# Kernel optimization log

Measured on AMD Instinct MI355X. Metric: run time of the kernel, lower is better.

## Reference

```python
import jax, jax.numpy as jnp
import numpy as np

C, FF, NH = 128, 2048, 8
B, D, H, W = 1, 16, 16, 16
EPS = 1e-5

def setup_inputs() -> dict:
    key = jax.random.key(0)
    ks = jax.random.split(key, 20)
    s = 0.02
    inp = {
        'x': jax.random.normal(ks[0], (B, C, D, H, W), jnp.float32),
        'Wq': jax.random.normal(ks[1], (C, C), jnp.float32) * s,
        'bq': jnp.zeros((C,), jnp.float32),
        'Wk': jax.random.normal(ks[2], (C, C), jnp.float32) * s,
        'bk': jnp.zeros((C,), jnp.float32),
        'Wv': jax.random.normal(ks[3], (C, C), jnp.float32) * s,
        'bv': jnp.zeros((C,), jnp.float32),
        'Wo': jax.random.normal(ks[4], (C, C), jnp.float32) * s,
        'bo': jnp.zeros((C,), jnp.float32),
        'W1': jax.random.normal(ks[5], (FF, C), jnp.float32) * s,
        'b1': jnp.zeros((FF,), jnp.float32),
        'W2': jax.random.normal(ks[6], (C, FF), jnp.float32) * s,
        'b2': jnp.zeros((C,), jnp.float32),
        'g1': jnp.ones((C,), jnp.float32),
        'be1': jnp.zeros((C,), jnp.float32),
        'g2': jnp.ones((C,), jnp.float32),
        'be2': jnp.zeros((C,), jnp.float32),
    }
    return inp

def _layernorm(t, g, b):
    # normalize over last (channel) dim, biased variance like torch LayerNorm
    m = jnp.mean(t, axis=-1, keepdims=True)
    v = jnp.mean(jnp.square(t - m), axis=-1, keepdims=True)
    return (t - m) * jax.lax.rsqrt(v + EPS) * g + b

def reference(x, Wq, bq, Wk, bk, Wv, bv, Wo, bo, W1, b1, W2, b2, g1, be1, g2, be2):
    b_, c, d, h, w = x.shape
    n = d * h * w
    hd = c // NH
    xf = x.reshape(b_, c, n)  # [B,C,N]
    # 1x1 conv3d == per-voxel linear over channels
    q = jnp.einsum('oc,bcn->bon', Wq, xf) + bq[:, None]
    k = jnp.einsum('oc,bcn->bon', Wk, xf) + bk[:, None]
    v = jnp.einsum('oc,bcn->bon', Wv, xf) + bv[:, None]
    q = q.reshape(b_, NH, hd, n)
    k = k.reshape(b_, NH, hd, n)
    v = v.reshape(b_, NH, hd, n)
    scores = jnp.einsum('bhcd,bhce->bhde', q, k) / (hd ** 0.5)  # [B,NH,N,N]
    probs = jax.nn.softmax(scores, axis=-1)
    attn = jnp.einsum('bhde,bhce->bhcd', probs, v).reshape(b_, c, n)
    attn = jnp.einsum('oc,bcn->bon', Wo, attn) + bo[:, None]
    x1 = xf + attn  # residual (dropout = identity at eval)
    x1 = _layernorm(x1.transpose(0, 2, 1), g1, be1)  # [B,N,C]
    hmid = jax.nn.relu(jnp.einsum('fc,bnc->bnf', W1, x1) + b1)
    ffn = jnp.einsum('cf,bnf->bnc', W2, hmid) + b2
    x2 = _layernorm(x1 + ffn, g2, be2)
    return x2.transpose(0, 2, 1).reshape(b_, c, d, h, w)
```

## Files before the change

kernel.cpp:

```cpp
#include <hip/hip_runtime.h>
#include <hip/hip_bf16.h>

typedef __hip_bfloat16 bf16;
typedef short short8 __attribute__((ext_vector_type(8)));
typedef float f32x4 __attribute__((ext_vector_type(4)));
typedef unsigned int u32x4 __attribute__((ext_vector_type(4)));

#define C_   128
#define N_   4096
#define NH_  8
#define HD_  16
#define FF_  2048
#define SCALE_Q 0.360673760222241f

__device__ __forceinline__ unsigned short f2bf_bits(float f) {
    bf16 h = __float2bfloat16(f);
    return *reinterpret_cast<unsigned short*>(&h);
}
__device__ __forceinline__ unsigned int pack_trunc(float lo, float hi) {
    return __builtin_amdgcn_perm(__float_as_uint(hi), __float_as_uint(lo), 0x07060302u);
}
__device__ __forceinline__ short f2bf_trunc(float f) {
    return (short)(__float_as_uint(f) >> 16);
}
__device__ __forceinline__ float bfs2f(short s) {
    return __uint_as_float(((unsigned int)(unsigned short)s) << 16);
}
__device__ __forceinline__ float fast_exp2(float x) {
    return __builtin_amdgcn_exp2f(x);
}
__device__ __forceinline__ f32x4 mfma16(short8 a, short8 b, f32x4 c) {
    return __builtin_amdgcn_mfma_f32_16x16x32_bf16(a, b, c, 0, 0, 0);
}

__global__ void __launch_bounds__(256) k_prep(
    const float* __restrict__ Wq, const float* __restrict__ Wk,
    const float* __restrict__ Wv, const float* __restrict__ Wo,
    const float* __restrict__ W1, const float* __restrict__ W2,
    const float* __restrict__ x,
    bf16* __restrict__ Wqkvf, bf16* __restrict__ Wof,
    bf16* __restrict__ W1f, bf16* __restrict__ W2f,
    bf16* __restrict__ xTf)
{
    const int i = blockIdx.x * 256 + threadIdx.x;
    if (i < 73728) {
        const float* row;
        bf16* dst;
        int kblk, g;
        if (i < 8192) {
            const int o = i >> 4;
            kblk = (i >> 2) & 3; g = i & 3;
            const int odx = (o < 384) ? o : o - 384;
            row = (o < 128) ? (Wq + o * 128)
                : (o < 256) ? (Wk + (o - 128) * 128)
                : (o < 384) ? (Wv + (o - 256) * 128)
                            : (Wo + (o - 384) * 128);
            bf16* buf = (o < 384) ? Wqkvf : Wof;
            dst = buf + ((((odx >> 4) << 2) + kblk) * 512 + ((g << 4) + (odx & 15)) * 8);
        } else if (i < 40960) {
            const int t = i - 8192, o = t >> 4;
            kblk = (t >> 2) & 3; g = t & 3;
            row = W1 + o * 128;
            dst = W1f + ((((o >> 4) << 2) + kblk) * 512 + ((g << 4) + (o & 15)) * 8);
        } else {
            const int t = i - 40960, o = t >> 8;
            kblk = (t >> 2) & 63; g = t & 3;
            row = W2 + o * 2048;
            dst = W2f + ((((o >> 4) << 6) + kblk) * 512 + ((g << 4) + (o & 15)) * 8);
        }
        const int k0 = kblk * 32 + g * 4;
        const f32x4 lo = *(const f32x4*)(row + k0);
        const f32x4 hi = *(const f32x4*)(row + k0 + 16);
        u32x4 w;
        #pragma unroll
        for (int j = 0; j < 4; ++j)
            w[j] = ((unsigned int)f2bf_bits(hi[j]) << 16) | f2bf_bits(lo[j]);
        *(u32x4*)dst = w;
    } else {
        const int t = i - 73728;
        const int n = t & 4095, g = (t >> 12) & 3, cblk = t >> 14;
        const int c0 = cblk * 32 + g * 4;
        const float* xs = x + (size_t)c0 * 4096 + n;
        u32x4 w;
        #pragma unroll
        for (int j = 0; j < 4; ++j)
            w[j] = ((unsigned int)f2bf_bits(xs[(size_t)(16 + j) * 4096]) << 16)
                 | f2bf_bits(xs[(size_t)j * 4096]);
        bf16* dst = xTf + ((((n >> 4) << 2) + cblk) * 512 + ((g << 4) + (n & 15)) * 8);
        *(u32x4*)dst = w;
    }
}

__global__ void __launch_bounds__(256) k_qkv(
    const bf16* __restrict__ xTf, const bf16* __restrict__ Wqkvf,
    const float* __restrict__ bq, const float* __restrict__ bk, const float* __restrict__ bv,
    bf16* __restrict__ qf, bf16* __restrict__ kf, bf16* __restrict__ vf)
{
    const int tid = threadIdx.x, wave = tid >> 6, lane = tid & 63;
    const int col = lane & 15, quad = lane >> 4;
    const int gw = blockIdx.x * 4 + wave;
    const int rt = gw / 24, ct = gw % 24;
    f32x4 acc = {};
    #pragma unroll
    for (int c = 0; c < 4; ++c) {
        short8 a = *(const short8*)(xTf + ((size_t)(rt * 4 + c) << 9) + lane * 8);
        short8 b = *(const short8*)(Wqkvf + ((size_t)(ct * 4 + c) << 9) + lane * 8);
        acc = mfma16(a, b, acc);
    }
    #pragma unroll
    for (int r = 0; r < 4; ++r) {
        const int m = rt * 16 + quad * 4 + r;
        const int n = ct * 16 + col;
        const float v = acc[r];
        if (n < 128) {
            const int h = n >> 4, ch = n & 15;
            qf[((h << 8) + (m >> 4)) * 256 + (((ch >> 3) << 4) + (m & 15)) * 8 + (ch & 7)] =
                __float2bfloat16((v + bq[n]) * SCALE_Q);
        } else if (n < 256) {
            const int c2 = n - 128, h = c2 >> 4, ch = c2 & 15;
            kf[((h << 8) + (m >> 4)) * 256 + (((ch >> 3) << 4) + (m & 15)) * 8 + (ch & 7)] =
                __float2bfloat16(v + bk[c2]);
        } else {
            const int c2 = n - 256, h = c2 >> 4, ch = c2 & 15;
            const int ko = m & 31;
            const int pos = ((ko & 15) << 1) + (ko >> 4);
            vf[((h << 7) + (m >> 5)) * 512 + (((pos >> 3) << 4) + ch) * 8 + (pos & 7)] =
                __float2bfloat16(v + bv[c2]);
        }
    }
}

__global__ void __launch_bounds__(256)
attn_kernel(const bf16* __restrict__ qf, const bf16* __restrict__ kf,
            const bf16* __restrict__ vf, bf16* __restrict__ af)
{
    __shared__ __align__(16) union {
        unsigned int P[4][4][2][320];
        float comb[4][4][64][8];
    } sh;
    const int tid = threadIdx.x, wave = tid >> 6, lane = tid & 63;
    const int col = lane & 15, quad = lane >> 4;
    const int gw = blockIdx.x;
    const int h  = gw >> 6;
    const int tile0 = (gw & 63) << 2;
    const f32x4 zero = {};

    short8 aq[4] = {{}, {}, {}, {}};
    if (quad < 2) {
        #pragma unroll
        for (int qt = 0; qt < 4; ++qt)
            aq[qt] = *(const short8*)(qf + ((size_t)((h << 8) + tile0 + qt) << 8) + lane * 8);
    }

    const short8 onesb = { (short)0x3F80, (short)0x3F80, (short)0x3F80, (short)0x3F80,
                           (short)0x3F80, (short)0x3F80, (short)0x3F80, (short)0x3F80 };

    f32x4 accO[4] = {{}, {}, {}, {}};
    f32x4 accL[4] = {{}, {}, {}, {}};

    const int kbeg = wave << 10;

    for (int i = 0; i < 32; i += 2) {
        const int mA = kbeg + (i << 5);
        const int mB = mA + 32;

        short8 bkA0 = {}, bkA1 = {}, bkB0 = {}, bkB1 = {};
        if (quad < 2) {
            const bf16* ka = kf + ((size_t)((h << 8) + (mA >> 4)) << 8) + lane * 8;
            bkA0 = *(const short8*)(ka);
            bkA1 = *(const short8*)(ka + 256);
            bkB0 = *(const short8*)(ka + 512);
            bkB1 = *(const short8*)(ka + 768);
        }
        const short8 vA = *(const short8*)(vf + ((size_t)((h << 7) + (mA >> 5)) << 9) + lane * 8);
        const short8 vB = *(const short8*)(vf + ((size_t)((h << 7) + (mB >> 5)) << 9) + lane * 8);

        #pragma unroll
        for (int qt = 0; qt < 4; ++qt) {
            f32x4 s0 = mfma16(aq[qt], bkA0, zero);
            f32x4 s1 = mfma16(aq[qt], bkA1, zero);
            f32x4 s2 = mfma16(aq[qt], bkB0, zero);
            f32x4 s3 = mfma16(aq[qt], bkB1, zero);
            unsigned int* P0 = &sh.P[wave][qt][0][0];
            unsigned int* P1 = &sh.P[wave][qt][1][0];
            #pragma unroll
            for (int r = 0; r < 4; ++r) {
                P0[(quad * 4 + r) * 20 + col] = pack_trunc(fast_exp2(s0[r]), fast_exp2(s1[r]));
                P1[(quad * 4 + r) * 20 + col] = pack_trunc(fast_exp2(s2[r]), fast_exp2(s3[r]));
            }
        }
        #pragma unroll
        for (int qt = 0; qt < 4; ++qt) {
            const short* Ps0 = (const short*)&sh.P[wave][qt][0][0];
            const short* Ps1 = (const short*)&sh.P[wave][qt][1][0];
            short8 ap0 = *(const short8*)(Ps0 + col * 40 + quad * 8);
            accO[qt] = mfma16(ap0, vA, accO[qt]);
            accL[qt] = mfma16(ap0, onesb, accL[qt]);
            short8 ap1 = *(const short8*)(Ps1 + col * 40 + quad * 8);
            accO[qt] = mfma16(ap1, vB, accO[qt]);
            accL[qt] = mfma16(ap1, onesb, accL[qt]);
        }
    }

    __syncthreads();
    #pragma unroll
    for (int qt = 0; qt < 4; ++qt)
        #pragma unroll
        for (int r = 0; r < 4; ++r) {
            sh.comb[qt][wave][lane][r]     = accO[qt][r];
            sh.comb[qt][wave][lane][4 + r] = accL[qt][r];
        }
    __syncthreads();

    {
        const int qt = wave, tile = tile0 + qt;
        #pragma unroll
        for (int r = 0; r < 4; ++r) {
            float O = sh.comb[qt][0][lane][r] + sh.comb[qt][1][lane][r]
                    + sh.comb[qt][2][lane][r] + sh.comb[qt][3][lane][r];
            float l = sh.comb[qt][0][lane][4+r] + sh.comb[qt][1][lane][4+r]
                    + sh.comb[qt][2][lane][4+r] + sh.comb[qt][3][lane][4+r];
            const int row16 = quad * 4 + r;
            const int pk = (col << 1) + (h & 1);
            af[((tile << 2) + (h >> 1)) * 512 + (((pk >> 3) << 4) + row16) * 8 + (pk & 7)] =
                __float2bfloat16(O / l);
        }
    }
}

__global__ void __launch_bounds__(512, 2)
k_mega(const bf16* __restrict__ af, const bf16* __restrict__ xTf,
       const bf16* __restrict__ Wof, const bf16* __restrict__ W1f, const bf16* __restrict__ W2f,
       const float* __restrict__ bo, const float* __restrict__ b1, const float* __restrict__ b2,
       const float* __restrict__ g1, const float* __restrict__ be1,
       const float* __restrict__ g2, const float* __restrict__ be2,
       float* __restrict__ out)
{
    __shared__ __align__(16) unsigned int Pb[8][2][320];
    __shared__ float comb[224][64];
    const int tid = threadIdx.x, wave = tid >> 6, lane = tid & 63;
    const int col = lane & 15, quad = lane >> 4;
    const int rt = blockIdx.x, n0 = rt << 4;
    const f32x4 zero = {};

    short8 ao[4], xt[4];
    #pragma unroll
    for (int c = 0; c < 4; ++c) {
        ao[c] = *(const short8*)(af  + ((size_t)(rt * 4 + c) << 9) + lane * 8);
        xt[c] = *(const short8*)(xTf + ((size_t)(rt * 4 + c) << 9) + lane * 8);
    }
    f32x4 d[8];
    #pragma unroll
    for (int t = 0; t < 8; ++t) d[t] = zero;
    #pragma unroll
    for (int t = 0; t < 8; ++t)
        #pragma unroll
        for (int c = 0; c < 4; ++c) {
            short8 b = *(const short8*)(Wof + ((size_t)(t * 4 + c) << 9) + lane * 8);
            d[t] = mfma16(ao[c], b, d[t]);
        }
    #pragma unroll
    for (int t = 0; t < 8; ++t) {
        const float bt = bo[t * 16 + col];
        #pragma unroll
        for (int r = 0; r < 4; ++r) d[t][r] += bt;
    }

    float x1f[4][8];
    #pragma unroll
    for (int c = 0; c < 4; ++c) {
        unsigned int* Pw = &Pb[wave][c & 1][0];
        const short* Ps = (const short*)Pw;
        #pragma unroll
        for (int r = 0; r < 4; ++r)
            Pw[(quad * 4 + r) * 20 + col] = pack_trunc(d[2 * c][r], d[2 * c + 1][r]);
        short8 ar = *(const short8*)(Ps + col * 40 + quad * 8);
        #pragma unroll
        for (int j = 0; j < 8; ++j)
            x1f[c][j] = bfs2f(ar[j]) + bfs2f(xt[c][j]);
    }

    float s = 0.f, ss = 0.f;
    #pragma unroll
    for (int c = 0; c < 4; ++c)
        #pragma unroll
        for (int j = 0; j < 8; ++j) { s += x1f[c][j]; ss += x1f[c][j] * x1f[c][j]; }
    s  += __shfl_xor(s, 16);  s  += __shfl_xor(s, 32);
    ss += __shfl_xor(ss, 16); ss += __shfl_xor(ss, 32);
    const float m1 = s * (1.f / 128.f);
    const float rstd1 = rsqrtf(ss * (1.f / 128.f) - m1 * m1 + 1e-5f);
    short8 aq1[4];
    #pragma unroll
    for (int c = 0; c < 4; ++c)
        #pragma unroll
        for (int j = 0; j < 8; ++j) {
            const int pos = quad * 8 + j;
            const int ko = ((pos & 1) << 4) + (pos >> 1);
            const int ch = c * 32 + ko;
            aq1[c][j] = f2bf_trunc((x1f[c][j] - m1) * rstd1 * g1[ch] + be1[ch]);
        }

    f32x4 ACC[8];
    #pragma unroll
    for (int t = 0; t < 8; ++t) ACC[t] = zero;
    for (int i = 0; i < 8; ++i) {
        const int ffc = (wave << 3) + i;
        f32x4 p0 = zero, p1 = zero;
        #pragma unroll
        for (int c = 0; c < 4; ++c) {
            short8 b = *(const short8*)(W1f + ((size_t)(ffc * 8 + c) << 9) + lane * 8);
            p0 = mfma16(aq1[c], b, p0);
        }
        #pragma unroll
        for (int c = 0; c < 4; ++c) {
            short8 b = *(const short8*)(W1f + ((size_t)(ffc * 8 + 4 + c) << 9) + lane * 8);
            p1 = mfma16(aq1[c], b, p1);
        }
        const float bb0 = b1[ffc * 32 + col], bb1 = b1[ffc * 32 + 16 + col];
        unsigned int* Pw = &Pb[wave][i & 1][0];
        #pragma unroll
        for (int r = 0; r < 4; ++r)
            Pw[(quad * 4 + r) * 20 + col] =
                pack_trunc(fmaxf(p0[r] + bb0, 0.f), fmaxf(p1[r] + bb1, 0.f));
        short8 ah = *(const short8*)((const short*)Pw + col * 40 + quad * 8);
        #pragma unroll
        for (int t = 0; t < 8; ++t) {
            short8 bw = *(const short8*)(W2f + ((size_t)(t * 64 + ffc) << 9) + lane * 8);
            ACC[t] = mfma16(ah, bw, ACC[t]);
        }
    }

    if (wave) {
        #pragma unroll
        for (int t = 0; t < 8; ++t)
            #pragma unroll
            for (int r = 0; r < 4; ++r)
                comb[(wave - 1) * 32 + t * 4 + r][lane] = ACC[t][r];
    }
    __syncthreads();
    if (wave == 0) {
        #pragma unroll
        for (int t = 0; t < 8; ++t)
            #pragma unroll
            for (int r = 0; r < 4; ++r) {
                float acc = ACC[t][r];
                #pragma unroll
                for (int w = 0; w < 7; ++w)
                    acc += comb[w * 32 + t * 4 + r][lane];
                ACC[t][r] = acc;
            }
        short* xb = (short*)&Pb[0][0][0];
        #pragma unroll
        for (int c = 0; c < 4; ++c)
            *(short8*)(xb + (col * 4 + c) * 32 + quad * 8) = aq1[c];
        float t2[8][4];
        #pragma unroll
        for (int t = 0; t < 8; ++t) {
            const int ch = t * 16 + col;
            const int pk = (col << 1) + (t & 1);
            const int c = t >> 1;
            const float bb = b2[ch];
            #pragma unroll
            for (int r = 0; r < 4; ++r)
                t2[t][r] = ACC[t][r] + bb + bfs2f(xb[((quad * 4 + r) * 4 + c) * 32 + pk]);
        }
        #pragma unroll
        for (int r = 0; r < 4; ++r) {
            float S = 0.f, SS = 0.f;
            #pragma unroll
            for (int t = 0; t < 8; ++t) { S += t2[t][r]; SS += t2[t][r] * t2[t][r]; }
            S  += __shfl_xor(S, 1);  S  += __shfl_xor(S, 2);
            S  += __shfl_xor(S, 4);  S  += __shfl_xor(S, 8);
            SS += __shfl_xor(SS, 1); SS += __shfl_xor(SS, 2);
            SS += __shfl_xor(SS, 4); SS += __shfl_xor(SS, 8);
            const float m2 = S * (1.f / 128.f);
            const float rstd2 = rsqrtf(SS * (1.f / 128.f) - m2 * m2 + 1e-5f);
            #pragma unroll
            for (int t = 0; t < 8; ++t) {
                const int ch = t * 16 + col;
                out[(size_t)ch * N_ + n0 + quad * 4 + r] =
                    (t2[t][r] - m2) * rstd2 * g2[ch] + be2[ch];
            }
        }
    }
}

extern "C" void kernel_launch(void* const* d_in, const int* in_sizes, int n_in,
                              void* d_out, int out_size, void* d_ws, size_t ws_size,
                              hipStream_t stream) {
    const float* x   = (const float*)d_in[0];
    const float* Wq  = (const float*)d_in[1];
    const float* bq  = (const float*)d_in[2];
    const float* Wk  = (const float*)d_in[3];
    const float* bk  = (const float*)d_in[4];
    const float* Wv  = (const float*)d_in[5];
    const float* bv  = (const float*)d_in[6];
    const float* Wo  = (const float*)d_in[7];
    const float* bo  = (const float*)d_in[8];
    const float* W1  = (const float*)d_in[9];
    const float* b1  = (const float*)d_in[10];
    const float* W2  = (const float*)d_in[11];
    const float* b2  = (const float*)d_in[12];
    const float* g1  = (const float*)d_in[13];
    const float* be1 = (const float*)d_in[14];
    const float* g2  = (const float*)d_in[15];
    const float* be2 = (const float*)d_in[16];
    float* out = (float*)d_out;

    char* ws = (char*)d_ws;
    bf16* xTf   = (bf16*)(ws + 0);
    bf16* qf    = (bf16*)(ws + 1048576);
    bf16* kf    = (bf16*)(ws + 2097152);
    bf16* vf    = (bf16*)(ws + 3145728);
    bf16* af    = (bf16*)(ws + 4194304);
    bf16* Wqkvf = (bf16*)(ws + 5242880);
    bf16* Wof   = (bf16*)(ws + 5341184);
    bf16* W1f   = (bf16*)(ws + 5373952);
    bf16* W2f   = (bf16*)(ws + 5898240);

    k_prep<<<544, 256, 0, stream>>>(Wq, Wk, Wv, Wo, W1, W2, x, Wqkvf, Wof, W1f, W2f, xTf);
    k_qkv<<<1536, 256, 0, stream>>>(xTf, Wqkvf, bq, bk, bv, qf, kf, vf);
    attn_kernel<<<512, 256, 0, stream>>>(qf, kf, vf, af);
    k_mega<<<256, 512, 0, stream>>>(af, xTf, Wof, W1f, W2f, bo, b1, b2,
                                    g1, be1, g2, be2, out);
}
```

Before: 139.2 us.

## Fuse all four kernels into one persistent kernel with grid-wide barriers

Replaces the four separate launches (prep, qkv, attention, mega) with a single persistent kernel of 256 blocks of 512 threads. The stages are separated by atomic-counter grid barriers, and a memset resets the counter before each launch. The W1/W2 weight conversion moves into the QKV stage so it overlaps with that work, and attention now runs two jobs per block. This removes launch gaps and tail effects between kernels, at the cost of barrier spin time, lower occupancy in the attention stage, and reliance on all 256 blocks being co-resident.

```diff
diff --git a/kernel.cpp b/kernel.cpp
--- a/kernel.cpp
+++ b/kernel.cpp
@@ -33,353 +33,379 @@
     return __builtin_amdgcn_mfma_f32_16x16x32_bf16(a, b, c, 0, 0, 0);
 }
 
-__global__ void __launch_bounds__(256) k_prep(
-    const float* __restrict__ Wq, const float* __restrict__ Wk,
-    const float* __restrict__ Wv, const float* __restrict__ Wo,
-    const float* __restrict__ W1, const float* __restrict__ W2,
-    const float* __restrict__ x,
-    bf16* __restrict__ Wqkvf, bf16* __restrict__ Wof,
-    bf16* __restrict__ W1f, bf16* __restrict__ W2f,
-    bf16* __restrict__ xTf)
+__device__ __forceinline__ void grid_sync(unsigned int* bar, unsigned int target) {
+    __syncthreads();
+    if (threadIdx.x == 0) {
+        __hip_atomic_fetch_add(bar, 1u, __ATOMIC_ACQ_REL, __HIP_MEMORY_SCOPE_AGENT);
+        while (__hip_atomic_load(bar, __ATOMIC_ACQUIRE, __HIP_MEMORY_SCOPE_AGENT) < target)
+            __builtin_amdgcn_s_sleep(2);
+    }
+    __syncthreads();
+}
+
+__global__ void __launch_bounds__(512)
+k_fused(const float* __restrict__ x,
+        const float* __restrict__ Wq, const float* __restrict__ Wk,
+        const float* __restrict__ Wv, const float* __restrict__ Wo,
+        const float* __restrict__ W1, const float* __restrict__ W2,
+        const float* __restrict__ bq, const float* __restrict__ bk,
+        const float* __restrict__ bv, const float* __restrict__ bo,
+        const float* __restrict__ b1, const float* __restrict__ b2,
+        const float* __restrict__ g1, const float* __restrict__ be1,
+        const float* __restrict__ g2, const float* __restrict__ be2,
+        bf16* __restrict__ xTf, bf16* __restrict__ Wqkvf, bf16* __restrict__ Wof,
+        bf16* __restrict__ W1f, bf16* __restrict__ W2f,
+        bf16* __restrict__ qf, bf16* __restrict__ kf, bf16* __restrict__ vf,
+        bf16* __restrict__ af,
+        float* __restrict__ out, unsigned int* __restrict__ bar)
 {
-    const int i = blockIdx.x * 256 + threadIdx.x;
-    if (i < 73728) {
-        const float* row;
-        bf16* dst;
-        int kblk, g;
+    __shared__ __align__(16) union {
+        unsigned int P[2][4][4][2][320];
+        float comba[2][4][4][64][8];
+        struct {
+            unsigned int Pb[8][2][320];
+            float comb[224][64];
+        } mg;
+    } sh;
+
+    const int tid  = threadIdx.x, wave = tid >> 6, lane = tid & 63;
+    const int col  = lane & 15,  quad = lane >> 4;
+    const int blk  = blockIdx.x;
+    const f32x4 zero = {};
+
+    {
+        const int i = blk * 512 + tid;
         if (i < 8192) {
             const int o = i >> 4;
-            kblk = (i >> 2) & 3; g = i & 3;
+            const int kblk = (i >> 2) & 3, g = i & 3;
             const int odx = (o < 384) ? o : o - 384;
-            row = (o < 128) ? (Wq + o * 128)
-                : (o < 256) ? (Wk + (o - 128) * 128)
-                : (o < 384) ? (Wv + (o - 256) * 128)
-                            : (Wo + (o - 384) * 128);
+            const float* row = (o < 128) ? (Wq + o * 128)
+                             : (o < 256) ? (Wk + (o - 128) * 128)
+                             : (o < 384) ? (Wv + (o - 256) * 128)
+                                         : (Wo + (o - 384) * 128);
             bf16* buf = (o < 384) ? Wqkvf : Wof;
-            dst = buf + ((((odx >> 4) << 2) + kblk) * 512 + ((g << 4) + (odx & 15)) * 8);
-        } else if (i < 40960) {
-            const int t = i - 8192, o = t >> 4;
-            kblk = (t >> 2) & 3; g = t & 3;
-            row = W1 + o * 128;
-            dst = W1f + ((((o >> 4) << 2) + kblk) * 512 + ((g << 4) + (o & 15)) * 8);
-        } else {
-            const int t = i - 40960, o = t >> 8;
-            kblk = (t >> 2) & 63; g = t & 3;
-            row = W2 + o * 2048;
-            dst = W2f + ((((o >> 4) << 6) + kblk) * 512 + ((g << 4) + (o & 15)) * 8);
-        }
-        const int k0 = kblk * 32 + g * 4;
-        const f32x4 lo = *(const f32x4*)(row + k0);
-        const f32x4 hi = *(const f32x4*)(row + k0 + 16);
-        u32x4 w;
-        #pragma unroll
-        for (int j = 0; j < 4; ++j)
-            w[j] = ((unsigned int)f2bf_bits(hi[j]) << 16) | f2bf_bits(lo[j]);
-        *(u32x4*)dst = w;
-    } else {
-        const int t = i - 73728;
-        const int n = t & 4095, g = (t >> 12) & 3, cblk = t >> 14;
-        const int c0 = cblk * 32 + g * 4;
-        const float* xs = x + (size_t)c0 * 4096 + n;
-        u32x4 w;
-        #pragma unroll
-        for (int j = 0; j < 4; ++j)
-            w[j] = ((unsigned int)f2bf_bits(xs[(size_t)(16 + j) * 4096]) << 16)
-                 | f2bf_bits(xs[(size_t)j * 4096]);
-        bf16* dst = xTf + ((((n >> 4) << 2) + cblk) * 512 + ((g << 4) + (n & 15)) * 8);
-        *(u32x4*)dst = w;
+            bf16* dst = buf + ((((odx >> 4) << 2) + kblk) * 512 + ((g << 4) + (odx & 15)) * 8);
+            const int k0 = kblk * 32 + g * 4;
+            const f32x4 lo = *(const f32x4*)(row + k0);
+            const f32x4 hi = *(const f32x4*)(row + k0 + 16);
+            u32x4 w;
+            #pragma unroll
+            for (int j = 0; j < 4; ++j)
+                w[j] = ((unsigned int)f2bf_bits(hi[j]) << 16) | f2bf_bits(lo[j]);
+            *(u32x4*)dst = w;
+        } else if (i < 73728) {
+            const int t = i - 8192;
+            const int n = t & 4095, g = (t >> 12) & 3, cblk = t >> 14;
+            const int c0 = cblk * 32 + g * 4;
+            const float* xs = x + (size_t)c0 * 4096 + n;
+            u32x4 w;
+            #pragma unroll
+            for (int j = 0; j < 4; ++j)
+                w[j] = ((unsigned int)f2bf_bits(xs[(size_t)(16 + j) * 4096]) << 16)
+                     | f2bf_bits(xs[(size_t)j * 4096]);
+            bf16* dst = xTf + ((((n >> 4) << 2) + cblk) * 512 + ((g << 4) + (n & 15)) * 8);
+            *(u32x4*)dst = w;
+        }
     }
-}
-
-__global__ void __launch_bounds__(256) k_qkv(
-    const bf16* __restrict__ xTf, const bf16* __restrict__ Wqkvf,
-    const float* __restrict__ bq, const float* __restrict__ bk, const float* __restrict__ bv,
-    bf16* __restrict__ qf, bf16* __restrict__ kf, bf16* __restrict__ vf)
-{
-    const int tid = threadIdx.x, wave = tid >> 6, lane = tid & 63;
-    const int col = lane & 15, quad = lane >> 4;
-    const int gw = blockIdx.x * 4 + wave;
-    const int rt = gw / 24, ct = gw % 24;
-    f32x4 acc = {};
-    #pragma unroll
-    for (int c = 0; c < 4; ++c) {
-        short8 a = *(const short8*)(xTf + ((size_t)(rt * 4 + c) << 9) + lane * 8);
-        short8 b = *(const short8*)(Wqkvf + ((size_t)(ct * 4 + c) << 9) + lane * 8);
-        acc = mfma16(a, b, acc);
+
+    grid_sync(bar, 256);
+
+    {
+        const int wv = blk * 8 + wave;
+        #pragma unroll
+        for (int j = 0; j < 3; ++j) {
+            const int gw = j * 2048 + wv;
+            const int rt = gw / 24, ct = gw % 24;
+            f32x4 acc = {};
+            #pragma unroll
+            for (int c = 0; c < 4; ++c) {
+                short8 a = *(const short8*)(xTf + ((size_t)(rt * 4 + c) << 9) + lane * 8);
+                short8 b = *(const short8*)(Wqkvf + ((size_t)(ct * 4 + c) << 9) + lane * 8);
+                acc = mfma16(a, b, acc);
+            }
+            #pragma unroll
+            for (int r = 0; r < 4; ++r) {
+                const int m = rt * 16 + quad * 4 + r;
+                const int n = ct * 16 + col;
+                const float v = acc[r];
+                if (n < 128) {
+                    const int h = n >> 4, ch = n & 15;
+                    qf[((h << 8) + (m >> 4)) * 256 + (((ch >> 3) << 4) + (m & 15)) * 8 + (ch & 7)] =
+                        __float2bfloat16((v + bq[n]) * SCALE_Q);
+                } else if (n < 256) {
+                    const int c2 = n - 128, h = c2 >> 4, ch = c2 & 15;
+                    kf[((h << 8) + (m >> 4)) * 256 + (((ch >> 3) << 4) + (m & 15)) * 8 + (ch & 7)] =
+                        __float2bfloat16(v + bk[c2]);
+                } else {
+                    const int c2 = n - 256, h = c2 >> 4, ch = c2 & 15;
+                    const int ko = m & 31;
+                    const int pos = ((ko & 15) << 1) + (ko >> 4);
+                    vf[((h << 7) + (m >> 5)) * 512 + (((pos >> 3) << 4) + ch) * 8 + (pos & 7)] =
+                        __float2bfloat16(v + bv[c2]);
+                }
+            }
+        }
+        const int i = blk * 512 + tid;
+        if (i < 65536) {
+            const float* row;
+            bf16* dst;
+            int kblk, g;
+            if (i < 32768) {
+                const int o = i >> 4;
+                kblk = (i >> 2) & 3; g = i & 3;
+                row = W1 + o * 128;
+                dst = W1f + ((((o >> 4) << 2) + kblk) * 512 + ((g << 4) + (o & 15)) * 8);
+            } else {
+                const int t = i - 32768, o = t >> 8;
+                kblk = (t >> 2) & 63; g = t & 3;
+                row = W2 + o * 2048;
+                dst = W2f + ((((o >> 4) << 6) + kblk) * 512 + ((g << 4) + (o & 15)) * 8);
+            }
+            const int k0 = kblk * 32 + g * 4;
+            const f32x4 lo = *(const f32x4*)(row + k0);
+            const f32x4 hi = *(const f32x4*)(row + k0 + 16);
+            u32x4 w;
+            #pragma unroll
+            for (int j = 0; j < 4; ++j)
+                w[j] = ((unsigned int)f2bf_bits(hi[j]) << 16) | f2bf_bits(lo[j]);
+            *(u32x4*)dst = w;
+        }
     }
-    #pragma unroll
-    for (int r = 0; r < 4; ++r) {
-        const int m = rt * 16 + quad * 4 + r;
-        const int n = ct * 16 + col;
-        const float v = acc[r];
-        if (n < 128) {
-            const int h = n >> 4, ch = n & 15;
-            qf[((h << 8) + (m >> 4)) * 256 + (((ch >> 3) << 4) + (m & 15)) * 8 + (ch & 7)] =
-                __float2bfloat16((v + bq[n]) * SCALE_Q);
-        } else if (n < 256) {
-            const int c2 = n - 128, h = c2 >> 4, ch = c2 & 15;
-            kf[((h << 8) + (m >> 4)) * 256 + (((ch >> 3) << 4) + (m & 15)) * 8 + (ch & 7)] =
-                __float2bfloat16(v + bk[c2]);
-        } else {
-            const int c2 = n - 256, h = c2 >> 4, ch = c2 & 15;
-            const int ko = m & 31;
-            const int pos = ((ko & 15) << 1) + (ko >> 4);
-            vf[((h << 7) + (m >> 5)) * 512 + (((pos >> 3) << 4) + ch) * 8 + (pos & 7)] =
-                __float2bfloat16(v + bv[c2]);
+
+    grid_sync(bar, 512);
+
+    {
+        const int half = wave >> 2, w4 = wave & 3;
+        const int job  = blk * 2 + half;
+        const int h    = job >> 6;
+        const int tile0 = (job & 63) << 2;
+
+        short8 aq[4] = {{}, {}, {}, {}};
+        if (quad < 2) {
+            #pragma unroll
+            for (int qt = 0; qt < 4; ++qt)
+                aq[qt] = *(const short8*)(qf + ((size_t)((h << 8) + tile0 + qt) << 8) + lane * 8);
+        }
+
+        const short8 onesb = { (short)0x3F80, (short)0x3F80, (short)0x3F80, (short)0x3F80,
+                               (short)0x3F80, (short)0x3F80, (short)0x3F80, (short)0x3F80 };
+
+        f32x4 accO[4] = {{}, {}, {}, {}};
+        f32x4 accL[4] = {{}, {}, {}, {}};
+
+        const int kbeg = w4 << 10;
+
+        for (int i = 0; i < 32; i += 2) {
+            const int mA = kbeg + (i << 5);
+            const int mB = mA + 32;
+
+            short8 bkA0 = {}, bkA1 = {}, bkB0 = {}, bkB1 = {};
+            if (quad < 2) {
+                const bf16* ka = kf + ((size_t)((h << 8) + (mA >> 4)) << 8) + lane * 8;
+                bkA0 = *(const short8*)(ka);
+                bkA1 = *(const short8*)(ka + 256);
+                bkB0 = *(const short8*)(ka + 512);
+                bkB1 = *(const short8*)(ka + 768);
+            }
+            const short8 vA = *(const short8*)(vf + ((size_t)((h << 7) + (mA >> 5)) << 9) + lane * 8);
+            const short8 vB = *(const short8*)(vf + ((size_t)((h << 7) + (mB >> 5)) << 9) + lane * 8);
+
+            #pragma unroll
+            for (int qt = 0; qt < 4; ++qt) {
+                f32x4 s0 = mfma16(aq[qt], bkA0, zero);
+                f32x4 s1 = mfma16(aq[qt], bkA1, zero);
+                f32x4 s2 = mfma16(aq[qt], bkB0, zero);
+                f32x4 s3 = mfma16(aq[qt], bkB1, zero);
+                unsigned int* P0 = &sh.P[half][w4][qt][0][0];
+                unsigned int* P1 = &sh.P[half][w4][qt][1][0];
+                #pragma unroll
+                for (int r = 0; r < 4; ++r) {
+                    P0[(quad * 4 + r) * 20 + col] = pack_trunc(fast_exp2(s0[r]), fast_exp2(s1[r]));
+                    P1[(quad * 4 + r) * 20 + col] = pack_trunc(fast_exp2(s2[r]), fast_exp2(s3[r]));
+                }
+            }
+            #pragma unroll
+            for (int qt = 0; qt < 4; ++qt) {
+                const short* Ps0 = (const short*)&sh.P[half][w4][qt][0][0];
+                const short* Ps1 = (const short*)&sh.P[half][w4][qt][1][0];
+                short8 ap0 = *(const short8*)(Ps0 + col * 40 + quad * 8);
+                accO[qt] = mfma16(ap0, vA, accO[qt]);
+                accL[qt] = mfma16(ap0, onesb, accL[qt]);
+                short8 ap1 = *(const short8*)(Ps1 + col * 40 + quad * 8);
+                accO[qt] = mfma16(ap1, vB, accO[qt]);
+                accL[qt] = mfma16(ap1, onesb, accL[qt]);
+            }
+        }
+
+        __syncthreads();
+        #pragma unroll
+        for (int qt = 0; qt < 4; ++qt)
+            #pragma unroll
+            for (int r = 0; r < 4; ++r) {
+                sh.comba[half][qt][w4][lane][r]     = accO[qt][r];
+                sh.comba[half][qt][w4][lane][4 + r] = accL[qt][r];
+            }
+        __syncthreads();
+
+        {
+            const int qt = w4, tile = tile0 + qt;
+            #pragma unroll
+            for (int r = 0; r < 4; ++r) {
+                float O = sh.comba[half][qt][0][lane][r] + sh.comba[half][qt][1][lane][r]
+                        + sh.comba[half][qt][2][lane][r] + sh.comba[half][qt][3][lane][r];
+                float l = sh.comba[half][qt][0][lane][4+r] + sh.comba[half][qt][1][lane][4+r]
+                        + sh.comba[half][qt][2][lane][4+r] + sh.comba[half][qt][3][lane][4+r];
+                const int row16 = quad * 4 + r;
+                const int pk = (col << 1) + (h & 1);
+                af[((tile << 2) + (h >> 1)) * 512 + (((pk >> 3) << 4) + row16) * 8 + (pk & 7)] =
+                    __float2bfloat16(O / l);
+            }
         }
     }
-}
-
-__global__ void __launch_bounds__(256)
-attn_kernel(const bf16* __restrict__ qf, const bf16* __restrict__ kf,
-            const bf16* __restrict__ vf, bf16* __restrict__ af)
-{
-    __shared__ __align__(16) union {
-        unsigned int P[4][4][2][320];
-        float comb[4][4][64][8];
-    } sh;
-    const int tid = threadIdx.x, wave = tid >> 6, lane = tid & 63;
-    const int col = lane & 15, quad = lane >> 4;
-    const int gw = blockIdx.x;
-    const int h  = gw >> 6;
-    const int tile0 = (gw & 63) << 2;
-    const f32x4 zero = {};
-
-    short8 aq[4] = {{}, {}, {}, {}};
-    if (quad < 2) {
-        #pragma unroll
-        for (int qt = 0; qt < 4; ++qt)
-            aq[qt] = *(const short8*)(qf + ((size_t)((h << 8) + tile0 + qt) << 8) + lane * 8);
-    }
-
-    const short8 onesb = { (short)0x3F80, (short)0x3F80, (short)0x3F80, (short)0x3F80,
-                           (short)0x3F80, (short)0x3F80, (short)0x3F80, (short)0x3F80 };
-
-    f32x4 accO[4] = {{}, {}, {}, {}};
-    f32x4 accL[4] = {{}, {}, {}, {}};
-
-    const int kbeg = wave << 10;
-
-    for (int i = 0; i < 32; i += 2) {
-        const int mA = kbeg + (i << 5);
-        const int mB = mA + 32;
-
-        short8 bkA0 = {}, bkA1 = {}, bkB0 = {}, bkB1 = {};
-        if (quad < 2) {
-            const bf16* ka = kf + ((size_t)((h << 8) + (mA >> 4)) << 8) + lane * 8;
-            bkA0 = *(const short8*)(ka);
-            bkA1 = *(const short8*)(ka + 256);
-            bkB0 = *(const short8*)(ka + 512);
-            bkB1 = *(const short8*)(ka + 768);
-        }
-        const short8 vA = *(const short8*)(vf + ((size_t)((h << 7) + (mA >> 5)) << 9) + lane * 8);
-        const short8 vB = *(const short8*)(vf + ((size_t)((h << 7) + (mB >> 5)) << 9) + lane * 8);
-
-        #pragma unroll
-        for (int qt = 0; qt < 4; ++qt) {
-            f32x4 s0 = mfma16(aq[qt], bkA0, zero);
-            f32x4 s1 = mfma16(aq[qt], bkA1, zero);
-            f32x4 s2 = mfma16(aq[qt], bkB0, zero);
-            f32x4 s3 = mfma16(aq[qt], bkB1, zero);
-            unsigned int* P0 = &sh.P[wave][qt][0][0];
-            unsigned int* P1 = &sh.P[wave][qt][1][0];
-            #pragma unroll
-            for (int r = 0; r < 4; ++r) {
-                P0[(quad * 4 + r) * 20 + col] = pack_trunc(fast_exp2(s0[r]), fast_exp2(s1[r]));
-                P1[(quad * 4 + r) * 20 + col] = pack_trunc(fast_exp2(s2[r]), fast_exp2(s3[r]));
-            }
-        }
-        #pragma unroll
-        for (int qt = 0; qt < 4; ++qt) {
-            const short* Ps0 = (const short*)&sh.P[wave][qt][0][0];
-            const short* Ps1 = (const short*)&sh.P[wave][qt][1][0];
-            short8 ap0 = *(const short8*)(Ps0 + col * 40 + quad * 8);
-            accO[qt] = mfma16(ap0, vA, accO[qt]);
-            accL[qt] = mfma16(ap0, onesb, accL[qt]);
-            short8 ap1 = *(const short8*)(Ps1 + col * 40 + quad * 8);
-            accO[qt] = mfma16(ap1, vB, accO[qt]);
-            accL[qt] = mfma16(ap1, onesb, accL[qt]);
-        }
-    }
-
-    __syncthreads();
-    #pragma unroll
-    for (int qt = 0; qt < 4; ++qt)
-        #pragma unroll
-        for (int r = 0; r < 4; ++r) {
-            sh.comb[qt][wave][lane][r]     = accO[qt][r];
-            sh.comb[qt][wave][lane][4 + r] = accL[qt][r];
-        }
-    __syncthreads();
+
+    grid_sync(bar, 768);
 
     {
-        const int qt = wave, tile = tile0 + qt;
-        #pragma unroll
-        for (int r = 0; r < 4; ++r) {
-            float O = sh.comb[qt][0][lane][r] + sh.comb[qt][1][lane][r]
-                    + sh.comb[qt][2][lane][r] + sh.comb[qt][3][lane][r];
-            float l = sh.comb[qt][0][lane][4+r] + sh.comb[qt][1][lane][4+r]
-                    + sh.comb[qt][2][lane][4+r] + sh.comb[qt][3][lane][4+r];
-            const int row16 = quad * 4 + r;
-            const int pk = (col << 1) + (h & 1);
-            af[((tile << 2) + (h >> 1)) * 512 + (((pk >> 3) << 4) + row16) * 8 + (pk & 7)] =
-                __float2bfloat16(O / l);
-        }
-    }
-}
-
-__global__ void __launch_bounds__(512, 2)
-k_mega(const bf16* __restrict__ af, const bf16* __restrict__ xTf,
-       const bf16* __restrict__ Wof, const bf16* __restrict__ W1f, const bf16* __restrict__ W2f,
-       const float* __restrict__ bo, const float* __restrict__ b1, const float* __restrict__ b2,
-       const float* __restrict__ g1, const float* __restrict__ be1,
-       const float* __restrict__ g2, const float* __restrict__ be2,
-       float* __restrict__ out)
-{
-    __shared__ __align__(16) unsigned int Pb[8][2][320];
-    __shared__ float comb[224][64];
-    const int tid = threadIdx.x, wave = tid >> 6, lane = tid & 63;
-    const int col = lane & 15, quad = lane >> 4;
-    const int rt = blockIdx.x, n0 = rt << 4;
-    const f32x4 zero = {};
-
-    short8 ao[4], xt[4];
-    #pragma unroll
-    for (int c = 0; c < 4; ++c) {
-        ao[c] = *(const short8*)(af  + ((size_t)(rt * 4 + c) << 9) + lane * 8);
-        xt[c] = *(const short8*)(xTf + ((size_t)(rt * 4 + c) << 9) + lane * 8);
-    }
-    f32x4 d[8];
-    #pragma unroll
-    for (int t = 0; t < 8; ++t) d[t] = zero;
-    #pragma unroll
-    for (int t = 0; t < 8; ++t)
+        const int rt = blk, n0 = rt << 4;
+
+        short8 ao[4], xt[4];
         #pragma unroll
         for (int c = 0; c < 4; ++c) {
-            short8 b = *(const short8*)(Wof + ((size_t)(t * 4 + c) << 9) + lane * 8);
-            d[t] = mfma16(ao[c], b, d[t]);
-        }
-    #pragma unroll
-    for (int t = 0; t < 8; ++t) {
-        const float bt = bo[t * 16 + col];
-        #pragma unroll
-        for (int r = 0; r < 4; ++r) d[t][r] += bt;
-    }
-
-    float x1f[4][8];
-    #pragma unroll
-    for (int c = 0; c < 4; ++c) {
-        unsigned int* Pw = &Pb[wave][c & 1][0];
-        const short* Ps = (const short*)Pw;
-        #pragma unroll
-        for (int r = 0; r < 4; ++r)
-            Pw[(quad * 4 + r) * 20 + col] = pack_trunc(d[2 * c][r], d[2 * c + 1][r]);
-        short8 ar = *(const short8*)(Ps + col * 40 + quad * 8);
-        #pragma unroll
-        for (int j = 0; j < 8; ++j)
-            x1f[c][j] = bfs2f(ar[j]) + bfs2f(xt[c][j]);
-    }
-
-    float s = 0.f, ss = 0.f;
-    #pragma unroll
-    for (int c = 0; c < 4; ++c)
-        #pragma unroll
-        for (int j = 0; j < 8; ++j) { s += x1f[c][j]; ss += x1f[c][j] * x1f[c][j]; }
-    s  += __shfl_xor(s, 16);  s  += __shfl_xor(s, 32);
-    ss += __shfl_xor(ss, 16); ss += __shfl_xor(ss, 32);
-    const float m1 = s * (1.f / 128.f);
-    const float rstd1 = rsqrtf(ss * (1.f / 128.f) - m1 * m1 + 1e-5f);
-    short8 aq1[4];
-    #pragma unroll
-    for (int c = 0; c < 4; ++c)
-        #pragma unroll
-        for (int j = 0; j < 8; ++j) {
-            const int pos = quad * 8 + j;
-            const int ko = ((pos & 1) << 4) + (pos >> 1);
-            const int ch = c * 32 + ko;
-            aq1[c][j] = f2bf_trunc((x1f[c][j] - m1) * rstd1 * g1[ch] + be1[ch]);
-        }
-
-    f32x4 ACC[8];
-    #pragma unroll
-    for (int t = 0; t < 8; ++t) ACC[t] = zero;
-    for (int i = 0; i < 8; ++i) {
-        const int ffc = (wave << 3) + i;
-        f32x4 p0 = zero, p1 = zero;
+            ao[c] = *(const short8*)(af  + ((size_t)(rt * 4 + c) << 9) + lane * 8);
+            xt[c] = *(const short8*)(xTf + ((size_t)(rt * 4 + c) << 9) + lane * 8);
+        }
+        f32x4 d[8];
+        #pragma unroll
+        for (int t = 0; t < 8; ++t) d[t] = zero;
+        #pragma unroll
+        for (int t = 0; t < 8; ++t)
+            #pragma unroll
+            for (int c = 0; c < 4; ++c) {
+                short8 b = *(const short8*)(Wof + ((size_t)(t * 4 + c) << 9) + lane * 8);
+                d[t] = mfma16(ao[c], b, d[t]);
+            }
+        #pragma unroll
+        for (int t = 0; t < 8; ++t) {
+            const float bt = bo[t * 16 + col];
+            #pragma unroll
+            for (int r = 0; r < 4; ++r) d[t][r] += bt;
+        }
+
+        float x1f[4][8];
         #pragma unroll
         for (int c = 0; c < 4; ++c) {
-            short8 b = *(const short8*)(W1f + ((size_t)(ffc * 8 + c) << 9) + lane * 8);
-            p0 = mfma16(aq1[c], b, p0);
-        }
-        #pragma unroll
-        for (int c = 0; c < 4; ++c) {
-            short8 b = *(const short8*)(W1f + ((size_t)(ffc * 8 + 4 + c) << 9) + lane * 8);
-            p1 = mfma16(aq1[c], b, p1);
-        }
-        const float bb0 = b1[ffc * 32 + col], bb1 = b1[ffc * 32 + 16 + col];
-        unsigned int* Pw = &Pb[wave][i & 1][0];
-        #pragma unroll
-        for (int r = 0; r < 4; ++r)
-            Pw[(quad * 4 + r) * 20 + col] =
-                pack_trunc(fmaxf(p0[r] + bb0, 0.f), fmaxf(p1[r] + bb1, 0.f));
-        short8 ah = *(const short8*)((const short*)Pw + col * 40 + quad * 8);
-        #pragma unroll
-        for (int t = 0; t < 8; ++t) {
-            short8 bw = *(const short8*)(W2f + ((size_t)(t * 64 + ffc) << 9) + lane * 8);
-            ACC[t] = mfma16(ah, bw, ACC[t]);
-        }
-    }
-
-    if (wave) {
-        #pragma unroll
-        for (int t = 0; t < 8; ++t)
+            unsigned int* Pw = &sh.mg.Pb[wave][c & 1][0];
+            const short* Ps = (const short*)Pw;
             #pragma unroll
             for (int r = 0; r < 4; ++r)
-                comb[(wave - 1) * 32 + t * 4 + r][lane] = ACC[t][r];
-    }
-    __syncthreads();
-    if (wave == 0) {
-        #pragma unroll
-        for (int t = 0; t < 8; ++t)
-            #pragma unroll
-            for (int r = 0; r < 4; ++r) {
-                float acc = ACC[t][r];
-                #pragma unroll
-                for (int w = 0; w < 7; ++w)
-                    acc += comb[w * 32 + t * 4 + r][lane];
-                ACC[t][r] = acc;
-            }
-        short* xb = (short*)&Pb[0][0][0];
+                Pw[(quad * 4 + r) * 20 + col] = pack_trunc(d[2 * c][r], d[2 * c + 1][r]);
+            short8 ar = *(const short8*)(Ps + col * 40 + quad * 8);
+            #pragma unroll
+            for (int j = 0; j < 8; ++j)
+                x1f[c][j] = bfs2f(ar[j]) + bfs2f(xt[c][j]);
+        }
+
+        float s = 0.f, ss = 0.f;
         #pragma unroll
         for (int c = 0; c < 4; ++c)
-            *(short8*)(xb + (col * 4 + c) * 32 + quad * 8) = aq1[c];
-        float t2[8][4];
-        #pragma unroll
-        for (int t = 0; t < 8; ++t) {
-            const int ch = t * 16 + col;
-            const int pk = (col << 1) + (t & 1);
-            const int c = t >> 1;
-            const float bb = b2[ch];
+            #pragma unroll
+            for (int j = 0; j < 8; ++j) { s += x1f[c][j]; ss += x1f[c][j] * x1f[c][j]; }
+        s  += __shfl_xor(s, 16);  s  += __shfl_xor(s, 32);
+        ss += __shfl_xor(ss, 16); ss += __shfl_xor(ss, 32);
+        const float m1 = s * (1.f / 128.f);
+        const float rstd1 = rsqrtf(ss * (1.f / 128.f) - m1 * m1 + 1e-5f);
+        short8 aq1[4];
+        #pragma unroll
+        for (int c = 0; c < 4; ++c)
+            #pragma unroll
+            for (int j = 0; j < 8; ++j) {
+                const int pos = quad * 8 + j;
+                const int ko = ((pos & 1) << 4) + (pos >> 1);
+                const int ch = c * 32 + ko;
+                aq1[c][j] = f2bf_trunc((x1f[c][j] - m1) * rstd1 * g1[ch] + be1[ch]);
+            }
+
+        f32x4 ACC[8];
+        #pragma unroll
+        for (int t = 0; t < 8; ++t) ACC[t] = zero;
+        for (int i = 0; i < 8; ++i) {
+            const int ffc = (wave << 3) + i;
+            f32x4 p0 = zero, p1 = zero;
+            #pragma unroll
+            for (int c = 0; c < 4; ++c) {
+                short8 b = *(const short8*)(W1f + ((size_t)(ffc * 8 + c) << 9) + lane * 8);
+                p0 = mfma16(aq1[c], b, p0);
+            }
+            #pragma unroll
+            for (int c = 0; c < 4; ++c) {
+                short8 b = *(const short8*)(W1f + ((size_t)(ffc * 8 + 4 + c) << 9) + lane * 8);
+                p1 = mfma16(aq1[c], b, p1);
+            }
+            const float bb0 = b1[ffc * 32 + col], bb1 = b1[ffc * 32 + 16 + col];
+            unsigned int* Pw = &sh.mg.Pb[wave][i & 1][0];
             #pragma unroll
             for (int r = 0; r < 4; ++r)
-                t2[t][r] = ACC[t][r] + bb + bfs2f(xb[((quad * 4 + r) * 4 + c) * 32 + pk]);
-        }
-        #pragma unroll
-        for (int r = 0; r < 4; ++r) {
-            float S = 0.f, SS = 0.f;
-            #pragma unroll
-            for (int t = 0; t < 8; ++t) { S += t2[t][r]; SS += t2[t][r] * t2[t][r]; }
-            S  += __shfl_xor(S, 1);  S  += __shfl_xor(S, 2);
-            S  += __shfl_xor(S, 4);  S  += __shfl_xor(S, 8);
-            SS += __shfl_xor(SS, 1); SS += __shfl_xor(SS, 2);
-            SS += __shfl_xor(SS, 4); SS += __shfl_xor(SS, 8);
-            const float m2 = S * (1.f / 128.f);
-            const float rstd2 = rsqrtf(SS * (1.f / 128.f) - m2 * m2 + 1e-5f);
+                Pw[(quad * 4 + r) * 20 + col] =
+                    pack_trunc(fmaxf(p0[r] + bb0, 0.f), fmaxf(p1[r] + bb1, 0.f));
+            short8 ah = *(const short8*)((const short*)Pw + col * 40 + quad * 8);
+            #pragma unroll
+            for (int t = 0; t < 8; ++t) {
+                short8 bw = *(const short8*)(W2f + ((size_t)(t * 64 + ffc) << 9) + lane * 8);
+                ACC[t] = mfma16(ah, bw, ACC[t]);
+            }
+        }
+
+        if (wave) {
+            #pragma unroll
+            for (int t = 0; t < 8; ++t)
+                #pragma unroll
+                for (int r = 0; r < 4; ++r)
+                    sh.mg.comb[(wave - 1) * 32 + t * 4 + r][lane] = ACC[t][r];
+        }
+        __syncthreads();
+        if (wave == 0) {
+            #pragma unroll
+            for (int t = 0; t < 8; ++t)
+                #pragma unroll
+                for (int r = 0; r < 4; ++r) {
+                    float acc = ACC[t][r];
+                    #pragma unroll
+                    for (int w = 0; w < 7; ++w)
+                        acc += sh.mg.comb[w * 32 + t * 4 + r][lane];
+                    ACC[t][r] = acc;
+                }
+            short* xb = (short*)&sh.mg.Pb[0][0][0];
+            #pragma unroll
+            for (int c = 0; c < 4; ++c)
+                *(short8*)(xb + (col * 4 + c) * 32 + quad * 8) = aq1[c];
+            float t2[8][4];
             #pragma unroll
             for (int t = 0; t < 8; ++t) {
                 const int ch = t * 16 + col;
-                out[(size_t)ch * N_ + n0 + quad * 4 + r] =
-                    (t2[t][r] - m2) * rstd2 * g2[ch] + be2[ch];
+                const int pk = (col << 1) + (t & 1);
+                const int c = t >> 1;
+                const float bb = b2[ch];
+                #pragma unroll
+                for (int r = 0; r < 4; ++r)
+                    t2[t][r] = ACC[t][r] + bb + bfs2f(xb[((quad * 4 + r) * 4 + c) * 32 + pk]);
+            }
+            #pragma unroll
+            for (int r = 0; r < 4; ++r) {
+                float S = 0.f, SS = 0.f;
+                #pragma unroll
+                for (int t = 0; t < 8; ++t) { S += t2[t][r]; SS += t2[t][r] * t2[t][r]; }
+                S  += __shfl_xor(S, 1);  S  += __shfl_xor(S, 2);
+                S  += __shfl_xor(S, 4);  S  += __shfl_xor(S, 8);
+                SS += __shfl_xor(SS, 1); SS += __shfl_xor(SS, 2);
+                SS += __shfl_xor(SS, 4); SS += __shfl_xor(SS, 8);
+                const float m2 = S * (1.f / 128.f);
+                const float rstd2 = rsqrtf(SS * (1.f / 128.f) - m2 * m2 + 1e-5f);
+                #pragma unroll
+                for (int t = 0; t < 8; ++t) {
+                    const int ch = t * 16 + col;
+                    out[(size_t)ch * N_ + n0 + quad * 4 + r] =
+                        (t2[t][r] - m2) * rstd2 * g2[ch] + be2[ch];
+                }
             }
         }
     }
@@ -417,10 +443,11 @@
     bf16* Wof   = (bf16*)(ws + 5341184);
     bf16* W1f   = (bf16*)(ws + 5373952);
     bf16* W2f   = (bf16*)(ws + 5898240);
-
-    k_prep<<<544, 256, 0, stream>>>(Wq, Wk, Wv, Wo, W1, W2, x, Wqkvf, Wof, W1f, W2f, xTf);
-    k_qkv<<<1536, 256, 0, stream>>>(xTf, Wqkvf, bq, bk, bv, qf, kf, vf);
-    attn_kernel<<<512, 256, 0, stream>>>(qf, kf, vf, af);
-    k_mega<<<256, 512, 0, stream>>>(af, xTf, Wof, W1f, W2f, bo, b1, b2,
-                                    g1, be1, g2, be2, out);
-}
+    unsigned int* bar = (unsigned int*)(ws + (8 << 20));
+
+    hipMemsetAsync(bar, 0, 256, stream);
+    k_fused<<<256, 512, 0, stream>>>(x, Wq, Wk, Wv, Wo, W1, W2,
+                                     bq, bk, bv, bo, b1, b2, g1, be1, g2, be2,
+                                     xTf, Wqkvf, Wof, W1f, W2f, qf, kf, vf, af,
+                                     out, bar);
+}
```

New measurement: 211.8 us. 52.1% more time.

## Split fused out-proj/FFN kernel into LN1, split-FF FFN, and reduce+LN2 kernels

Applied to the files above, without the earlier changes.

The single mega kernel (256 blocks, 8 waves each looping over the full FF dimension) becomes three kernels. One computes the output projection, residual and LayerNorm1 into a bf16 buffer. One splits the FF dimension 8 ways across 512 blocks and writes fp32 partial sums. A final kernel reduces the partials and applies LayerNorm2. This raises parallelism in the FFN, which previously had only 256 blocks on a 256-CU GPU, at the cost of two extra launches and about 16 MB of fp32 partial-sum traffic.

```diff
diff --git a/kernel.cpp b/kernel.cpp
--- a/kernel.cpp
+++ b/kernel.cpp
@@ -228,19 +228,16 @@
     }
 }
 
-__global__ void __launch_bounds__(512, 2)
-k_mega(const bf16* __restrict__ af, const bf16* __restrict__ xTf,
-       const bf16* __restrict__ Wof, const bf16* __restrict__ W1f, const bf16* __restrict__ W2f,
-       const float* __restrict__ bo, const float* __restrict__ b1, const float* __restrict__ b2,
-       const float* __restrict__ g1, const float* __restrict__ be1,
-       const float* __restrict__ g2, const float* __restrict__ be2,
-       float* __restrict__ out)
-{
-    __shared__ __align__(16) unsigned int Pb[8][2][320];
-    __shared__ float comb[224][64];
+__global__ void __launch_bounds__(256)
+k_ln1(const bf16* __restrict__ af, const bf16* __restrict__ xTf,
+      const bf16* __restrict__ Wof, const float* __restrict__ bo,
+      const float* __restrict__ g1, const float* __restrict__ be1,
+      bf16* __restrict__ x1qf)
+{
+    __shared__ __align__(16) unsigned int Pb[4][2][320];
     const int tid = threadIdx.x, wave = tid >> 6, lane = tid & 63;
     const int col = lane & 15, quad = lane >> 4;
-    const int rt = blockIdx.x, n0 = rt << 4;
+    const int rt = blockIdx.x;
     const f32x4 zero = {};
 
     short8 ao[4], xt[4];
@@ -289,22 +286,48 @@
     ss += __shfl_xor(ss, 16); ss += __shfl_xor(ss, 32);
     const float m1 = s * (1.f / 128.f);
     const float rstd1 = rsqrtf(ss * (1.f / 128.f) - m1 * m1 + 1e-5f);
-    short8 aq1[4];
-    #pragma unroll
-    for (int c = 0; c < 4; ++c)
+    #pragma unroll
+    for (int c = 0; c < 4; ++c) {
+        short8 aq1;
         #pragma unroll
         for (int j = 0; j < 8; ++j) {
             const int pos = quad * 8 + j;
             const int ko = ((pos & 1) << 4) + (pos >> 1);
             const int ch = c * 32 + ko;
-            aq1[c][j] = f2bf_trunc((x1f[c][j] - m1) * rstd1 * g1[ch] + be1[ch]);
-        }
+            aq1[j] = f2bf_trunc((x1f[c][j] - m1) * rstd1 * g1[ch] + be1[ch]);
+        }
+        if (wave == 0)
+            *(short8*)((short*)x1qf + ((size_t)(rt * 4 + c) << 9) + lane * 8) = aq1;
+    }
+}
+
+__global__ void __launch_bounds__(512, 4)
+k_ffn(const bf16* __restrict__ x1qf, const bf16* __restrict__ W1f,
+      const bf16* __restrict__ W2f, const float* __restrict__ b1,
+      const float* __restrict__ b2, float* __restrict__ partial)
+{
+    __shared__ __align__(16) unsigned int Pb[8][2][320];
+    __shared__ float comb[4][32][64];
+    __shared__ short xb[4][2048];
+    const int tid = threadIdx.x, wave = tid >> 6, lane = tid & 63;
+    const int col = lane & 15, quad = lane >> 4;
+    const int blk = blockIdx.x;
+    const int fq = blk & 7, nt = blk >> 3;
+    const int rt_l = wave & 3, chalf = wave >> 2;
+    const int grt = nt * 4 + rt_l, n0 = grt << 4;
+    const f32x4 zero = {};
+
+    short8 aq1[4];
+    #pragma unroll
+    for (int c = 0; c < 4; ++c)
+        aq1[c] = *(const short8*)((const short*)x1qf + ((size_t)(grt * 4 + c) << 9) + lane * 8);
 
     f32x4 ACC[8];
     #pragma unroll
     for (int t = 0; t < 8; ++t) ACC[t] = zero;
-    for (int i = 0; i < 8; ++i) {
-        const int ffc = (wave << 3) + i;
+    #pragma unroll
+    for (int i = 0; i < 4; ++i) {
+        const int ffc = fq * 8 + chalf * 4 + i;
         f32x4 p0 = zero, p1 = zero;
         #pragma unroll
         for (int c = 0; c < 4; ++c) {
@@ -330,58 +353,79 @@
         }
     }
 
-    if (wave) {
+    if (wave >= 4) {
         #pragma unroll
         for (int t = 0; t < 8; ++t)
             #pragma unroll
             for (int r = 0; r < 4; ++r)
-                comb[(wave - 1) * 32 + t * 4 + r][lane] = ACC[t][r];
+                comb[wave - 4][t * 4 + r][lane] = ACC[t][r];
     }
     __syncthreads();
-    if (wave == 0) {
+    if (wave < 4) {
         #pragma unroll
         for (int t = 0; t < 8; ++t)
             #pragma unroll
-            for (int r = 0; r < 4; ++r) {
-                float acc = ACC[t][r];
-                #pragma unroll
-                for (int w = 0; w < 7; ++w)
-                    acc += comb[w * 32 + t * 4 + r][lane];
-                ACC[t][r] = acc;
-            }
-        short* xb = (short*)&Pb[0][0][0];
-        #pragma unroll
-        for (int c = 0; c < 4; ++c)
-            *(short8*)(xb + (col * 4 + c) * 32 + quad * 8) = aq1[c];
-        float t2[8][4];
-        #pragma unroll
-        for (int t = 0; t < 8; ++t) {
-            const int ch = t * 16 + col;
-            const int pk = (col << 1) + (t & 1);
-            const int c = t >> 1;
-            const float bb = b2[ch];
-            #pragma unroll
             for (int r = 0; r < 4; ++r)
-                t2[t][r] = ACC[t][r] + bb + bfs2f(xb[((quad * 4 + r) * 4 + c) * 32 + pk]);
-        }
-        #pragma unroll
-        for (int r = 0; r < 4; ++r) {
-            float S = 0.f, SS = 0.f;
-            #pragma unroll
-            for (int t = 0; t < 8; ++t) { S += t2[t][r]; SS += t2[t][r] * t2[t][r]; }
-            S  += __shfl_xor(S, 1);  S  += __shfl_xor(S, 2);
-            S  += __shfl_xor(S, 4);  S  += __shfl_xor(S, 8);
-            SS += __shfl_xor(SS, 1); SS += __shfl_xor(SS, 2);
-            SS += __shfl_xor(SS, 4); SS += __shfl_xor(SS, 8);
-            const float m2 = S * (1.f / 128.f);
-            const float rstd2 = rsqrtf(SS * (1.f / 128.f) - m2 * m2 + 1e-5f);
+                ACC[t][r] += comb[wave][t * 4 + r][lane];
+
+        float* pdst = partial + ((size_t)fq << 19);
+        if (fq == 0) {
+            short* x = &xb[wave][0];
+            #pragma unroll
+            for (int c = 0; c < 4; ++c)
+                *(short8*)(x + (col * 4 + c) * 32 + quad * 8) = aq1[c];
             #pragma unroll
             for (int t = 0; t < 8; ++t) {
                 const int ch = t * 16 + col;
-                out[(size_t)ch * N_ + n0 + quad * 4 + r] =
-                    (t2[t][r] - m2) * rstd2 * g2[ch] + be2[ch];
+                const int pk = (col << 1) + (t & 1);
+                const int c = t >> 1;
+                const float bb = b2[ch];
+                #pragma unroll
+                for (int r = 0; r < 4; ++r)
+                    pdst[(size_t)(n0 + quad * 4 + r) * 128 + ch] =
+                        ACC[t][r] + bb + bfs2f(x[((quad * 4 + r) * 4 + c) * 32 + pk]);
             }
-        }
+        } else {
+            #pragma unroll
+            for (int t = 0; t < 8; ++t) {
+                const int ch = t * 16 + col;
+                #pragma unroll
+                for (int r = 0; r < 4; ++r)
+                    pdst[(size_t)(n0 + quad * 4 + r) * 128 + ch] = ACC[t][r];
+            }
+        }
+    }
+}
+
+__global__ void __launch_bounds__(512)
+k_fin(const float* __restrict__ partial, const float* __restrict__ g2,
+      const float* __restrict__ be2, float* __restrict__ out)
+{
+    const int tid = threadIdx.x;
+    const int cq = tid & 31, ri = tid >> 5;
+    const int n = blockIdx.x * 16 + ri;
+
+    const float* ps = partial + (size_t)n * 128 + cq * 4;
+    f32x4 v = {};
+    #pragma unroll
+    for (int fq = 0; fq < 8; ++fq) {
+        const f32x4 p = *(const f32x4*)(ps + ((size_t)fq << 19));
+        #pragma unroll
+        for (int k = 0; k < 4; ++k) v[k] += p[k];
+    }
+    float S = 0.f, SS = 0.f;
+    #pragma unroll
+    for (int k = 0; k < 4; ++k) { S += v[k]; SS += v[k] * v[k]; }
+    S  += __shfl_xor(S, 1);  S  += __shfl_xor(S, 2);
+    S  += __shfl_xor(S, 4);  S  += __shfl_xor(S, 8);  S  += __shfl_xor(S, 16);
+    SS += __shfl_xor(SS, 1); SS += __shfl_xor(SS, 2);
+    SS += __shfl_xor(SS, 4); SS += __shfl_xor(SS, 8); SS += __shfl_xor(SS, 16);
+    const float m2 = S * (1.f / 128.f);
+    const float rstd2 = rsqrtf(SS * (1.f / 128.f) - m2 * m2 + 1e-5f);
+    #pragma unroll
+    for (int k = 0; k < 4; ++k) {
+        const int ch = cq * 4 + k;
+        out[(size_t)ch * N_ + n] = (v[k] - m2) * rstd2 * g2[ch] + be2[ch];
     }
 }
 
@@ -417,10 +461,13 @@
     bf16* Wof   = (bf16*)(ws + 5341184);
     bf16* W1f   = (bf16*)(ws + 5373952);
     bf16* W2f   = (bf16*)(ws + 5898240);
+    bf16* x1qf  = (bf16*)(ws + 6422528);
+    float* partial = (float*)(ws + 7471104);
 
     k_prep<<<544, 256, 0, stream>>>(Wq, Wk, Wv, Wo, W1, W2, x, Wqkvf, Wof, W1f, W2f, xTf);
     k_qkv<<<1536, 256, 0, stream>>>(xTf, Wqkvf, bq, bk, bv, qf, kf, vf);
     attn_kernel<<<512, 256, 0, stream>>>(qf, kf, vf, af);
-    k_mega<<<256, 512, 0, stream>>>(af, xTf, Wof, W1f, W2f, bo, b1, b2,
-                                    g1, be1, g2, be2, out);
-}
+    k_ln1<<<256, 256, 0, stream>>>(af, xTf, Wof, bo, g1, be1, x1qf);
+    k_ffn<<<512, 512, 0, stream>>>(x1qf, W1f, W2f, b1, b2, partial);
+    k_fin<<<256, 512, 0, stream>>>(partial, g2, be2, out);
+}
```

Result: slower. 145.9 us (+4.8%).
